# Performance work log

Hardware: AMD Instinct MI355X
Metric: run time of the kernel (lower is better)

The kernel has to match this reference:

```python
import jax, jax.numpy as jnp
import numpy as np

B, L, D = 8, 128, 768  # batch, max_len, in_features == out_features


def setup_inputs() -> dict:
    key = jax.random.key(0)
    k1, k2, k3, k4, k5 = jax.random.split(key, 5)
    text = jax.random.normal(k1, (B, L, D), dtype=jnp.float32)
    adj = jax.random.uniform(k2, (B, L, L), dtype=jnp.float32)
    dep_embed = jax.random.normal(k3, (B, L, L, D), dtype=jnp.float32)
    # kaiming_uniform-ish init scale for weight, small bias
    bound_w = 1.0 / np.sqrt(D)
    weight = jax.random.uniform(k4, (D, D), minval=-bound_w, maxval=bound_w, dtype=jnp.float32)
    bias = jax.random.uniform(k5, (D,), minval=-bound_w, maxval=bound_w, dtype=jnp.float32)
    return {"text": text, "adj": adj, "dep_embed": dep_embed, "weight": weight, "bias": bias}


def reference(text, adj, dep_embed, weight, bias):
    # Original math: out[b,i,:] = relu(sum_j adj[b,i,j] * ((text[b,j]+dep_embed[b,j,i]) @ W) + bias)
    # Fused form: aggregate first (linear in j), then apply the single GEMM with W.
    agg = jnp.einsum('bij,bjd->bid', adj, text)              # neighbor-sum of node feats
    agg = agg + jnp.einsum('bij,bjid->bid', adj, dep_embed)  # neighbor-sum of edge-type embeds
    out = jnp.einsum('bid,de->bie', agg, weight) + bias
    return jax.nn.relu(out)
```

## Files before the change

### kernel.cpp

```cpp
#include <hip/hip_runtime.h>

#define B_ 8
#define L_ 128
#define D_ 768

__global__ __launch_bounds__(192) void agg_kernel(
    const float* __restrict__ text,
    const float* __restrict__ adj,
    const float* __restrict__ dep,
    float* __restrict__ agg) {
  const int bi = blockIdx.x;
  const int b  = bi >> 7;
  const int i  = bi & (L_ - 1);
  const int t  = threadIdx.x;

  __shared__ float adj_s[L_];
  if (t < L_) adj_s[t] = adj[(size_t)bi * L_ + t];
  __syncthreads();

  const float4* text4 = (const float4*)(text + (size_t)b * L_ * D_);
  const float4* dep4  = (const float4*)(dep + ((size_t)(b * L_) * L_ + i) * D_);

  float4 acc = make_float4(0.f, 0.f, 0.f, 0.f);
#pragma unroll 4
  for (int j = 0; j < L_; ++j) {
    const float  a  = adj_s[j];
    const float4 tx = text4[j * (D_ / 4) + t];
    const float4 dv = dep4[(size_t)j * (L_ * D_ / 4) + t];
    acc.x += a * (tx.x + dv.x);
    acc.y += a * (tx.y + dv.y);
    acc.z += a * (tx.z + dv.z);
    acc.w += a * (tx.w + dv.w);
  }
  ((float4*)(agg + (size_t)bi * D_))[t] = acc;
}

#define TM 64
#define TN 64
#define TK 32

__global__ __launch_bounds__(256) void gemm_bias_relu(
    const float* __restrict__ A,
    const float* __restrict__ W,
    const float* __restrict__ bias,
    float* __restrict__ out) {
  __shared__ float As[TM][TK + 4];
  __shared__ float Bs[TK][TN];

  const int tid = threadIdx.x;
  const int tx  = tid & 15;
  const int ty  = tid >> 4;
  const int m0  = blockIdx.y * TM;
  const int n0  = blockIdx.x * TN;

  const int ar = tid >> 3;
  const int ac = (tid & 7) * 4;
  const int br = tid >> 4;
  const int bc = (tid & 15) * 4;

  float acc[4][4] = {};

  for (int k0 = 0; k0 < D_; k0 += TK) {
    const float4 a0 = *(const float4*)&A[(size_t)(m0 + ar) * D_ + k0 + ac];
    const float4 a1 = *(const float4*)&A[(size_t)(m0 + ar + 32) * D_ + k0 + ac];
    const float4 b0 = *(const float4*)&W[(size_t)(k0 + br) * D_ + n0 + bc];
    const float4 b1 = *(const float4*)&W[(size_t)(k0 + br + 16) * D_ + n0 + bc];
    __syncthreads();
    *(float4*)&As[ar][ac]       = a0;
    *(float4*)&As[ar + 32][ac]  = a1;
    *(float4*)&Bs[br][bc]       = b0;
    *(float4*)&Bs[br + 16][bc]  = b1;
    __syncthreads();

#pragma unroll
    for (int kk = 0; kk < TK; ++kk) {
      float av[4];
#pragma unroll
      for (int p = 0; p < 4; ++p) av[p] = As[ty * 4 + p][kk];
      const float4 bv = *(const float4*)&Bs[kk][tx * 4];
      const float bb[4] = {bv.x, bv.y, bv.z, bv.w};
#pragma unroll
      for (int pm = 0; pm < 4; ++pm)
#pragma unroll
        for (int pn = 0; pn < 4; ++pn)
          acc[pm][pn] += av[pm] * bb[pn];
    }
  }

  const float4 bvec = *(const float4*)&bias[n0 + tx * 4];
  const float bias4[4] = {bvec.x, bvec.y, bvec.z, bvec.w};
#pragma unroll
  for (int pm = 0; pm < 4; ++pm) {
    float4 o;
    o.x = fmaxf(acc[pm][0] + bias4[0], 0.f);
    o.y = fmaxf(acc[pm][1] + bias4[1], 0.f);
    o.z = fmaxf(acc[pm][2] + bias4[2], 0.f);
    o.w = fmaxf(acc[pm][3] + bias4[3], 0.f);
    *(float4*)&out[(size_t)(m0 + ty * 4 + pm) * D_ + n0 + tx * 4] = o;
  }
}

extern "C" void kernel_launch(void* const* d_in, const int* in_sizes, int n_in,
                              void* d_out, int out_size, void* d_ws, size_t ws_size,
                              hipStream_t stream) {
  const float* text   = (const float*)d_in[0];
  const float* adj    = (const float*)d_in[1];
  const float* dep    = (const float*)d_in[2];
  const float* weight = (const float*)d_in[3];
  const float* bias   = (const float*)d_in[4];
  float* out = (float*)d_out;
  float* agg = (float*)d_ws;

  agg_kernel<<<B_ * L_, 192, 0, stream>>>(text, adj, dep, agg);

  dim3 grid(D_ / TN, (B_ * L_) / TM);
  gemm_bias_relu<<<grid, 256, 0, stream>>>(agg, weight, bias, out);
}
```

Measured before the change: 559.9 us.

## Use nontemporal dep loads, wider unroll, and a prefetched transposed GEMM tile

```diff
diff --git a/kernel.cpp b/kernel.cpp
--- a/kernel.cpp
+++ b/kernel.cpp
@@ -3,6 +3,8 @@
 #define B_ 8
 #define L_ 128
 #define D_ 768
+
+typedef float v4f __attribute__((ext_vector_type(4)));
 
 __global__ __launch_bounds__(192) void agg_kernel(
     const float* __restrict__ text,
@@ -18,33 +20,31 @@
   if (t < L_) adj_s[t] = adj[(size_t)bi * L_ + t];
   __syncthreads();
 
-  const float4* text4 = (const float4*)(text + (size_t)b * L_ * D_);
-  const float4* dep4  = (const float4*)(dep + ((size_t)(b * L_) * L_ + i) * D_);
+  const v4f* text4 = (const v4f*)(text + (size_t)b * L_ * D_);
+  const v4f* dep4  = (const v4f*)(dep + ((size_t)(b * L_) * L_ + i) * D_);
 
-  float4 acc = make_float4(0.f, 0.f, 0.f, 0.f);
-#pragma unroll 4
+  v4f acc = {0.f, 0.f, 0.f, 0.f};
+#pragma unroll 8
   for (int j = 0; j < L_; ++j) {
-    const float  a  = adj_s[j];
-    const float4 tx = text4[j * (D_ / 4) + t];
-    const float4 dv = dep4[(size_t)j * (L_ * D_ / 4) + t];
-    acc.x += a * (tx.x + dv.x);
-    acc.y += a * (tx.y + dv.y);
-    acc.z += a * (tx.z + dv.z);
-    acc.w += a * (tx.w + dv.w);
+    const float a  = adj_s[j];
+    const v4f   tx = text4[j * (D_ / 4) + t];
+    const v4f   dv = __builtin_nontemporal_load(&dep4[(size_t)j * (L_ * D_ / 4) + t]);
+    acc += a * (tx + dv);
   }
-  ((float4*)(agg + (size_t)bi * D_))[t] = acc;
+  ((v4f*)(agg + (size_t)bi * D_))[t] = acc;
 }
 
-#define TM 64
+#define TM 32
 #define TN 64
 #define TK 32
+#define NKT (D_ / TK)
 
 __global__ __launch_bounds__(256) void gemm_bias_relu(
     const float* __restrict__ A,
     const float* __restrict__ W,
     const float* __restrict__ bias,
     float* __restrict__ out) {
-  __shared__ float As[TM][TK + 4];
+  __shared__ float AsT[TK][TM + 2];
   __shared__ float Bs[TK][TN];
 
   const int tid = threadIdx.x;
@@ -53,50 +53,56 @@
   const int m0  = blockIdx.y * TM;
   const int n0  = blockIdx.x * TN;
 
-  const int ar = tid >> 3;
-  const int ac = (tid & 7) * 4;
-  const int br = tid >> 4;
-  const int bc = (tid & 15) * 4;
+  const int ar  = tid >> 3;
+  const int ac  = (tid & 7) * 4;
+  const int br  = tid >> 4;
+  const int bc  = (tid & 15) * 4;
 
-  float acc[4][4] = {};
+  const float* Arow = A + (size_t)(m0 + ar) * D_ + ac;
+  const float* Wrow0 = W + (size_t)br * D_ + n0 + bc;
+  const float* Wrow1 = W + (size_t)(br + 16) * D_ + n0 + bc;
 
-  for (int k0 = 0; k0 < D_; k0 += TK) {
-    const float4 a0 = *(const float4*)&A[(size_t)(m0 + ar) * D_ + k0 + ac];
-    const float4 a1 = *(const float4*)&A[(size_t)(m0 + ar + 32) * D_ + k0 + ac];
-    const float4 b0 = *(const float4*)&W[(size_t)(k0 + br) * D_ + n0 + bc];
-    const float4 b1 = *(const float4*)&W[(size_t)(k0 + br + 16) * D_ + n0 + bc];
+  float acc[2][4] = {};
+
+  v4f a_reg  = *(const v4f*)Arow;
+  v4f b_reg0 = *(const v4f*)Wrow0;
+  v4f b_reg1 = *(const v4f*)Wrow1;
+
+  for (int t = 0; t < NKT; ++t) {
     __syncthreads();
-    *(float4*)&As[ar][ac]       = a0;
-    *(float4*)&As[ar + 32][ac]  = a1;
-    *(float4*)&Bs[br][bc]       = b0;
-    *(float4*)&Bs[br + 16][bc]  = b1;
+    AsT[ac + 0][ar] = a_reg.x;
+    AsT[ac + 1][ar] = a_reg.y;
+    AsT[ac + 2][ar] = a_reg.z;
+    AsT[ac + 3][ar] = a_reg.w;
+    *(v4f*)&Bs[br][bc]      = b_reg0;
+    *(v4f*)&Bs[br + 16][bc] = b_reg1;
     __syncthreads();
+
+    if (t + 1 < NKT) {
+      a_reg  = *(const v4f*)(Arow + (t + 1) * TK);
+      b_reg0 = *(const v4f*)(Wrow0 + (size_t)(t + 1) * TK * D_);
+      b_reg1 = *(const v4f*)(Wrow1 + (size_t)(t + 1) * TK * D_);
+    }
 
 #pragma unroll
     for (int kk = 0; kk < TK; ++kk) {
-      float av[4];
+      const float2 av = *(const float2*)&AsT[kk][ty * 2];
+      const v4f    bv = *(const v4f*)&Bs[kk][tx * 4];
 #pragma unroll
-      for (int p = 0; p < 4; ++p) av[p] = As[ty * 4 + p][kk];
-      const float4 bv = *(const float4*)&Bs[kk][tx * 4];
-      const float bb[4] = {bv.x, bv.y, bv.z, bv.w};
-#pragma unroll
-      for (int pm = 0; pm < 4; ++pm)
-#pragma unroll
-        for (int pn = 0; pn < 4; ++pn)
-          acc[pm][pn] += av[pm] * bb[pn];
+      for (int pn = 0; pn < 4; ++pn) {
+        acc[0][pn] += av.x * bv[pn];
+        acc[1][pn] += av.y * bv[pn];
+      }
     }
   }
 
-  const float4 bvec = *(const float4*)&bias[n0 + tx * 4];
-  const float bias4[4] = {bvec.x, bvec.y, bvec.z, bvec.w};
+  const v4f bvec = *(const v4f*)&bias[n0 + tx * 4];
 #pragma unroll
-  for (int pm = 0; pm < 4; ++pm) {
-    float4 o;
-    o.x = fmaxf(acc[pm][0] + bias4[0], 0.f);
-    o.y = fmaxf(acc[pm][1] + bias4[1], 0.f);
-    o.z = fmaxf(acc[pm][2] + bias4[2], 0.f);
-    o.w = fmaxf(acc[pm][3] + bias4[3], 0.f);
-    *(float4*)&out[(size_t)(m0 + ty * 4 + pm) * D_ + n0 + tx * 4] = o;
+  for (int pm = 0; pm < 2; ++pm) {
+    v4f o;
+#pragma unroll
+    for (int pn = 0; pn < 4; ++pn) o[pn] = fmaxf(acc[pm][pn] + bvec[pn], 0.f);
+    *(v4f*)&out[(size_t)(m0 + ty * 2 + pm) * D_ + n0 + tx * 4] = o;
   }
 }
 
```

Measured after the change: 545.6 us. 2.6% less time.
